# Optimization experiments

Measured on AMD Instinct MI355X. Metric: run time of the kernel, lower is better.

The kernel has to match this reference:

```python
import jax, jax.numpy as jnp
import numpy as np

FP, DP, K, S, B, T, H, ZD = 96, 28, 3, 4, 64, 8, 512, 2
CP = FP - DP + 1          # 69, valid cross-correlation output size
NP = CP * CP              # 4761 = num_pixels


def setup_inputs() -> dict:
    key = jax.random.key(0)
    ks = jax.random.split(key, 12)
    def rn(k, shape, s=0.02):
        return jax.random.normal(k, shape, jnp.float32) * s
    return {
        "frames": jax.random.uniform(ks[0], (S, B, T, FP, FP), jnp.float32),
        "conv_kernel": jax.random.uniform(ks[1], (S, B, K, DP, DP), jnp.float32),
        "eps": jax.random.normal(ks[2], (S, B, K, ZD), jnp.float32),
        "W1": rn(ks[3], (NP, H)), "b1": jnp.zeros((H,), jnp.float32),
        "Wm1": rn(ks[4], (H, H // 2)), "bm1": jnp.zeros((H // 2,), jnp.float32),
        "Wm2": rn(ks[5], (H // 2, ZD)), "bm2": jnp.zeros((ZD,), jnp.float32),
        "Ws1": rn(ks[6], (H, H // 2)), "bs1": jnp.zeros((H // 2,), jnp.float32),
        "Ws2": rn(ks[7], (H // 2, ZD)), "bs2": jnp.zeros((ZD,), jnp.float32),
        "timestep": 0,
    }


def _axis_weights(p, n):
    """Bilinear 1-D gather indices/weights with zero padding outside [0, n)."""
    p0 = jnp.floor(p)
    f = p - p0
    i0 = p0.astype(jnp.int32)
    i1 = i0 + 1
    w0 = jnp.where((i0 >= 0) & (i0 < n), 1.0 - f, 0.0)
    w1 = jnp.where((i1 >= 0) & (i1 < n), f, 0.0)
    return jnp.clip(i0, 0, n - 1), jnp.clip(i1, 0, n - 1), w0, w1


def _place_digit(digit, zw):
    """AT.digit_to_frame: place DPxDP digit into FPxFP frame at z_where (torch
    affine_grid/grid_sample, align_corners=False, zero padding). theta scale =
    FP/DP, translation = -z_where*FP/DP, i.e. in_coord = (FP/DP)*(out - zw)."""
    scale = FP / DP
    out_c = (2.0 * jnp.arange(FP, dtype=jnp.float32) + 1.0) / FP - 1.0  # (FP,)
    px = ((scale * (out_c - zw[0]) + 1.0) * DP - 1.0) * 0.5  # x source pix
    py = ((scale * (out_c - zw[1]) + 1.0) * DP - 1.0) * 0.5  # y source pix
    y0, y1, wy0, wy1 = _axis_weights(py, DP)
    x0, x1, wx0, wx1 = _axis_weights(px, DP)
    # separable bilinear: interp rows then cols
    tmp = wy0[:, None] * digit[y0, :] + wy1[:, None] * digit[y1, :]  # (FP,DP)
    return wx0[None, :] * tmp[:, x0] + wx1[None, :] * tmp[:, x1]     # (FP,FP)

_place_batch = jax.vmap(_place_digit)


def reference(frames, conv_kernel, eps, W1, b1, Wm1, bm1, Wm2, bm2,
              Ws1, bs1, Ws2, bs2, timestep):
    SB = S * B
    frame_left = frames[:, :, timestep]  # (S,B,FP,FP)
    means, stds, zs = [], [], []
    for k in range(K):
        # per-sample dynamic-kernel cross-correlation via grouped conv
        lhs = frame_left.reshape(1, SB, FP, FP)
        rhs = conv_kernel[:, :, k].reshape(SB, 1, DP, DP)
        conved = jax.lax.conv_general_dilated(
            lhs, rhs, (1, 1), 'VALID', feature_group_count=SB)  # (1,SB,CP,CP)
        scores = jax.nn.softmax(conved.reshape(S, B, NP), axis=-1)
        h = jax.nn.relu(scores @ W1 + b1)                       # (S,B,H)
        mean_k = jnp.tanh(jax.nn.relu(h @ Wm1 + bm1) @ Wm2 + bm2)
        std_k = jnp.exp(jax.nn.relu(h @ Ws1 + bs1) @ Ws2 + bs2)
        z_k = mean_k + std_k * eps[:, :, k]                     # rsample
        recon = _place_batch(conv_kernel[:, :, k].reshape(SB, DP, DP),
                             z_k.reshape(SB, ZD)).reshape(S, B, FP, FP)
        frame_left = frame_left - recon
        means.append(mean_k); stds.append(std_k); zs.append(z_k)
    q_mean = jnp.stack(means, 2)    # (S,B,K,2)
    q_std = jnp.stack(stds, 2)
    z_where = jnp.stack(zs, 2)
    return jnp.stack([q_mean, q_std, z_where], 0)  # (3,S,B,K,2)
```

## Files before the change

kernel.cpp:

```cpp
#include <hip/hip_runtime.h>
#include <hip/hip_bf16.h>
#include <math.h>

#define FPD 96
#define DPD 28
#define CPD 69
#define NPD 4761
#define KKC 3
#define SBN 256
#define TT 8
#define HD 512
#define ZDD 2
#define KPAD 4768
#define SPLITK 15
#define FRSH 104
#define CVS 76

typedef __attribute__((ext_vector_type(8))) short bf16x8;
typedef __attribute__((ext_vector_type(4))) float f32x4;
typedef _Float16 half_t;
typedef __attribute__((ext_vector_type(2))) _Float16 half2_t;

__device__ __forceinline__ float bf2f_lo(unsigned int u) {
    union { unsigned int i; float f; } v; v.i = u << 16; return v.f;
}
__device__ __forceinline__ float bf2f_hi(unsigned int u) {
    union { unsigned int i; float f; } v; v.i = u & 0xffff0000u; return v.f;
}
__device__ __forceinline__ half2_t u2h(unsigned int u) {
    union { unsigned int i; half2_t h; } v; v.i = u; return v.h;
}

struct ConvLds {
    half_t fr[96 * FRSH];
    half_t kr[28 * 32];
    float  dg[784];
    float  cv[4][69 * CVS];
    float  red[32];
};

struct MlpLds {
    float hsh[HD];
    float h2[2][256];
    float res_sh[2][2];
};

__device__ __forceinline__ void conv_rest(
    ConvLds& L, int k, int ib, int t,
    const float* __restrict__ pf,
    float* __restrict__ frameL,
    float zx, float zy,
    ushort* __restrict__ e_buf, float* __restrict__ inv_denom)
{
    half_t* fr  = L.fr;
    half_t* kr  = L.kr;
    float*  dg  = L.dg;
    float*  red = L.red;

    const float scale = 96.f / 28.f;
    #pragma unroll
    for (int i = 0; i < 9; ++i) {
        int p = t + i * 1024;
        int r = p / 96, c = p - r * 96;
        float val = pf[i];
        if (k > 0) {
            float oci = (2.f * r + 1.f) / 96.f - 1.f;
            float ocj = (2.f * c + 1.f) / 96.f - 1.f;
            float py = ((scale * (oci - zy) + 1.f) * 28.f - 1.f) * 0.5f;
            float px = ((scale * (ocj - zx) + 1.f) * 28.f - 1.f) * 0.5f;
            float py0f = floorf(py), px0f = floorf(px);
            float fy = py - py0f, fx = px - px0f;
            int y0 = (int)py0f, x0 = (int)px0f;
            int y1 = y0 + 1, x1 = x0 + 1;
            float wy0 = (y0 >= 0 && y0 < DPD) ? 1.f - fy : 0.f;
            float wy1 = (y1 >= 0 && y1 < DPD) ? fy : 0.f;
            float wx0 = (x0 >= 0 && x0 < DPD) ? 1.f - fx : 0.f;
            float wx1 = (x1 >= 0 && x1 < DPD) ? fx : 0.f;
            int y0c = min(max(y0, 0), DPD - 1), y1c = min(max(y1, 0), DPD - 1);
            int x0c = min(max(x0, 0), DPD - 1), x1c = min(max(x1, 0), DPD - 1);
            float tmp0 = wy0 * dg[y0c * DPD + x0c] + wy1 * dg[y1c * DPD + x0c];
            float tmp1 = wy0 * dg[y0c * DPD + x1c] + wy1 * dg[y1c * DPD + x1c];
            val -= wx0 * tmp0 + wx1 * tmp1;
        }
        fr[r * FRSH + c] = (half_t)val;
        if (k == 1) frameL[(size_t)ib * 9216 + p] = val;
    }
    if (t < 96 * 8) fr[(t >> 3) * FRSH + 96 + (t & 7)] = (half_t)0.f;
    __syncthreads();

    if (t < 828) {
        const int q    = t / 207;
        const int rem  = t - q * 207;
        const int tile = rem / 69;
        const int oy   = rem - tile * 69;
        const int ox0  = tile * 24;
        const int dy0  = q * 7;

        float acc[24];
        #pragma unroll
        for (int j = 0; j < 24; ++j) acc[j] = 0.f;

        #pragma unroll 1
        for (int dd = 0; dd < 7; ++dd) {
            const int dy = dy0 + dd;
            const unsigned int* frow = (const unsigned int*)&fr[(oy + dy) * FRSH + ox0];
            const unsigned int* krow = (const unsigned int*)&kr[dy * 32];
            unsigned int W[28], K[16], V[25];
            #pragma unroll
            for (int u = 0; u < 7; ++u) {
                uint4 v = *(const uint4*)(frow + 4 * u);
                W[4*u] = v.x; W[4*u+1] = v.y; W[4*u+2] = v.z; W[4*u+3] = v.w;
            }
            #pragma unroll
            for (int u = 0; u < 4; ++u) {
                uint4 v = *(const uint4*)(krow + 4 * u);
                K[4*u] = v.x; K[4*u+1] = v.y; K[4*u+2] = v.z; K[4*u+3] = v.w;
            }
            #pragma unroll
            for (int i = 0; i < 25; ++i)
                V[i] = (W[i] >> 16) | (W[i + 1] << 16);
            #pragma unroll
            for (int m = 0; m < 12; ++m) {
                float ae = acc[2*m], ao = acc[2*m+1];
                #pragma unroll
                for (int i = 0; i < 14; ++i) {
                    ae = __builtin_amdgcn_fdot2(u2h(W[m + i]), u2h(K[i]), ae, false);
                    ao = __builtin_amdgcn_fdot2(u2h(V[m + i]), u2h(K[i]), ao, false);
                }
                acc[2*m] = ae; acc[2*m+1] = ao;
            }
        }
        float* cvq = &L.cv[q][oy * CVS + ox0];
        #pragma unroll
        for (int u = 0; u < 6; ++u) {
            float4 v = make_float4(acc[4*u], acc[4*u+1], acc[4*u+2], acc[4*u+3]);
            *(float4*)(cvq + 4 * u) = v;
        }
    }
    __syncthreads();

    float m = -INFINITY;
    for (int p = t; p < 69 * CVS; p += 1024) {
        int ox = p - (p / CVS) * CVS;
        if (ox < CPD) {
            float v = L.cv[0][p] + L.cv[1][p] + L.cv[2][p] + L.cv[3][p];
            L.cv[0][p] = v;
            m = fmaxf(m, v);
        }
    }
    #pragma unroll
    for (int off = 32; off > 0; off >>= 1) m = fmaxf(m, __shfl_down(m, off, 64));
    int lane = t & 63, wid = t >> 6;
    if (lane == 0) red[wid] = m;
    __syncthreads();
    m = red[0];
    #pragma unroll
    for (int i = 1; i < 16; ++i) m = fmaxf(m, red[i]);

    float s = 0.f;
    ushort* eo = e_buf + (size_t)ib * KPAD;
    for (int p = t; p < 69 * CVS; p += 1024) {
        int oy = p / CVS;
        int ox = p - oy * CVS;
        if (ox < CPD) {
            float ev = __expf(L.cv[0][p] - m);
            __hip_bfloat16 h = __float2bfloat16(ev);
            eo[oy * CPD + ox] = *reinterpret_cast<ushort*>(&h);
            s += ev;
        }
    }
    #pragma unroll
    for (int off = 32; off > 0; off >>= 1) s += __shfl_down(s, off, 64);
    if (lane == 0) red[16 + wid] = s;
    __syncthreads();
    if (t == 0) {
        float tot = 0.f;
        #pragma unroll
        for (int i = 0; i < 16; ++i) tot += red[16 + i];
        inv_denom[ib] = 1.0f / tot;
    }
    if (t < KPAD - NPD) eo[NPD + t] = 0;
}

__device__ __forceinline__ void mlp_phase(
    MlpLds& L, int km, int ib, int t,
    float csum, float invd, float b1v,
    const ushort* __restrict__ WhidT,
    const float* __restrict__ bm1, const float* __restrict__ bs1,
    const float* __restrict__ Wm2, const float* __restrict__ bm2,
    const float* __restrict__ Ws2, const float* __restrict__ bs2,
    const float* __restrict__ eps, float* __restrict__ out,
    float* z_keep)
{
    if (t < HD)
        L.hsh[t] = fmaxf(fmaf(csum, invd, b1v), 0.f);
    __syncthreads();

    if (t < 512) {
        int head = t >> 8, col = t & 255;
        const uint4* Wr = (const uint4*)(WhidT + (size_t)(head * 256 + col) * 512);
        float bias = head ? bs1[col] : bm1[col];
        float a = 0.f;
        #pragma unroll 8
        for (int u = 0; u < 64; ++u) {
            uint4 wv = Wr[u];
            const float* hp = &L.hsh[u * 8];
            a = fmaf(hp[0], bf2f_lo(wv.x), a);
            a = fmaf(hp[1], bf2f_hi(wv.x), a);
            a = fmaf(hp[2], bf2f_lo(wv.y), a);
            a = fmaf(hp[3], bf2f_hi(wv.y), a);
            a = fmaf(hp[4], bf2f_lo(wv.z), a);
            a = fmaf(hp[5], bf2f_hi(wv.z), a);
            a = fmaf(hp[6], bf2f_lo(wv.w), a);
            a = fmaf(hp[7], bf2f_hi(wv.w), a);
        }
        L.h2[head][col] = fmaxf(a + bias, 0.f);
    }
    __syncthreads();

    {
        int w = t >> 6, l = t & 63;
        if (w < 4) {
            int zd = (w >> 1) & 1, head = w & 1;
            const float* W2 = head ? Ws2 : Wm2;
            float a = 0.f;
            #pragma unroll
            for (int u = 0; u < 4; ++u) {
                int i = l + u * 64;
                a = fmaf(L.h2[head][i], W2[i * 2 + zd], a);
            }
            #pragma unroll
            for (int off = 32; off > 0; off >>= 1) a += __shfl_down(a, off, 64);
            if (l == 0) {
                float r = head ? __expf(a + bs2[zd]) : tanhf(a + bm2[zd]);
                L.res_sh[zd][head] = r;
            }
        }
    }
    __syncthreads();
    if (t < 2) {
        int zd = t;
        float mean = L.res_sh[zd][0];
        float stdv = L.res_sh[zd][1];
        float ev = eps[(size_t)ib * 6 + km * 2 + zd];
        float z = fmaf(stdv, ev, mean);
        int oidx = ib * 6 + km * 2 + zd;
        out[oidx]        = mean;
        out[1536 + oidx] = stdv;
        out[3072 + oidx] = z;
        z_keep[zd] = z;
    }
}

__global__
__attribute__((amdgpu_flat_work_group_size(1024, 1024)))
__attribute__((amdgpu_waves_per_eu(4, 4)))
void conv0_wprep_kernel(
    const float* __restrict__ frames, const int* __restrict__ tsp,
    float* __restrict__ frameL, const float* __restrict__ ck,
    ushort* __restrict__ e_buf, float* __restrict__ inv_denom,
    const float* __restrict__ W1, const float* __restrict__ Wm1,
    const float* __restrict__ Ws1,
    ushort* __restrict__ W1T, ushort* __restrict__ WhidT)
{
    __shared__ union __align__(16) {
        ConvLds conv;
        ushort wp[4][64][65];
    } sh;
    const int t  = threadIdx.x;
    const int ib = blockIdx.x;

    const float* src = frames + ((size_t)ib * TT + *tsp) * 9216;
    float pf[9];
    #pragma unroll
    for (int i = 0; i < 9; ++i) pf[i] = src[t + i * 1024];
    if (t < 28 * 32) {
        int dy = t >> 5, dx = t & 31;
        float v = (dx < 28) ? ck[((size_t)ib * KKC + 0) * 784 + dy * 28 + dx] : 0.f;
        sh.conv.kr[t] = (half_t)v;
    }

    conv_rest(sh.conv, 0, ib, t, pf, frameL, 0.f, 0.f, e_buf, inv_denom);
    __syncthreads();

    {
        const int g  = t >> 8;
        const int tt = t & 255;
        const int ln = tt & 63;
        const int lr = tt >> 6;
        const int b  = ib * 4 + g;
        ushort (*tile)[65] = sh.wp[g];

        if (b < 600) {
            const int k0 = (b % 75) * 64;
            const int n0 = (b / 75) * 64;
            #pragma unroll
            for (int i = 0; i < 16; ++i) {
                int kk = k0 + lr + i * 4;
                float v = (kk < NPD) ? W1[(size_t)kk * HD + n0 + ln] : 0.f;
                __hip_bfloat16 h = __float2bfloat16(v);
                tile[lr + i * 4][ln] = *reinterpret_cast<ushort*>(&h);
            }
        } else if (b < 664) {
            const int bb = b - 600;
            const int i0 = (bb & 7) * 64;
            const int r0 = (bb >> 3) * 64;
            #pragma unroll
            for (int rep = 0; rep < 16; ++rep) {
                int i = i0 + lr + rep * 4;
                int r = r0 + ln;
                const float* srcp = (r >= 256) ? Ws1 : Wm1;
                float v = srcp[(size_t)i * 256 + (r & 255)];
                __hip_bfloat16 h = __float2bfloat16(v);
                tile[lr + rep * 4][ln] = *reinterpret_cast<ushort*>(&h);
            }
        }
        __syncthreads();
        if (b < 600) {
            const int k0 = (b % 75) * 64;
            const int n0 = (b / 75) * 64;
            #pragma unroll
            for (int i = 0; i < 16; ++i) {
                int nn = lr + i * 4;
                int kk = k0 + ln;
                if (kk < KPAD)
                    W1T[(size_t)(n0 + nn) * KPAD + kk] = tile[ln][nn];
            }
        } else if (b < 664) {
            const int bb = b - 600;
            const int i0 = (bb & 7) * 64;
            const int r0 = (bb >> 3) * 64;
            #pragma unroll
            for (int rep = 0; rep < 16; ++rep) {
                int r = r0 + lr + rep * 4;
                WhidT[(size_t)r * 512 + i0 + ln] = tile[ln][lr + rep * 4];
            }
        }
    }
}

__global__ __launch_bounds__(256) void gemm1_mfma(
    const ushort* __restrict__ E, const ushort* __restrict__ W1T,
    float* __restrict__ Cpart)
{
    const int t  = threadIdx.x;
    const int m0 = blockIdx.x * 64;
    const int n0 = blockIdx.y * 64;
    const int z  = blockIdx.z;
    const int step0 = z * 10;
    const int nstep = min(10, 149 - step0);

    const int l  = t & 63;
    const int w  = t >> 6;
    const int lm = l & 15;
    const int kb = l >> 4;

    f32x4 zero = {0.f, 0.f, 0.f, 0.f};
    f32x4 acc[4] = {zero, zero, zero, zero};

    const ushort* pA = E   + (size_t)(m0 + w * 16 + lm) * KPAD + kb * 8;
    const ushort* pB = W1T + (size_t)(n0 + lm) * KPAD + kb * 8;

    int kk = step0 * 32;
    bf16x8 a  = *(const bf16x8*)(pA + kk);
    bf16x8 b0 = *(const bf16x8*)(pB + kk);
    bf16x8 b1 = *(const bf16x8*)(pB + 16 * KPAD + kk);
    bf16x8 b2 = *(const bf16x8*)(pB + 32 * KPAD + kk);
    bf16x8 b3 = *(const bf16x8*)(pB + 48 * KPAD + kk);

    for (int s = 0; s < nstep; ++s) {
        bf16x8 ca = a, c0 = b0, c1 = b1, c2 = b2, c3 = b3;
        if (s + 1 < nstep) {
            kk += 32;
            a  = *(const bf16x8*)(pA + kk);
            b0 = *(const bf16x8*)(pB + kk);
            b1 = *(const bf16x8*)(pB + 16 * KPAD + kk);
            b2 = *(const bf16x8*)(pB + 32 * KPAD + kk);
            b3 = *(const bf16x8*)(pB + 48 * KPAD + kk);
        }
        acc[0] = __builtin_amdgcn_mfma_f32_16x16x32_bf16(ca, c0, acc[0], 0, 0, 0);
        acc[1] = __builtin_amdgcn_mfma_f32_16x16x32_bf16(ca, c1, acc[1], 0, 0, 0);
        acc[2] = __builtin_amdgcn_mfma_f32_16x16x32_bf16(ca, c2, acc[2], 0, 0, 0);
        acc[3] = __builtin_amdgcn_mfma_f32_16x16x32_bf16(ca, c3, acc[3], 0, 0, 0);
    }

    const int mrow = m0 + w * 16 + kb * 4;
    #pragma unroll
    for (int j = 0; j < 4; ++j) {
        int n = n0 + j * 16 + lm;
        #pragma unroll
        for (int rg = 0; rg < 4; ++rg)
            Cpart[((size_t)(mrow + rg) * SPLITK + z) * HD + n] = acc[j][rg];
    }
}

__global__
__attribute__((amdgpu_flat_work_group_size(1024, 1024)))
__attribute__((amdgpu_waves_per_eu(4, 4)))
void mlp_conv_kernel(
    const float* __restrict__ Cpart, const float* __restrict__ inv_denom,
    const float* __restrict__ b1, const ushort* __restrict__ WhidT,
    const float* __restrict__ bm1, const float* __restrict__ bs1,
    const float* __restrict__ Wm2, const float* __restrict__ bm2,
    const float* __restrict__ Ws2, const float* __restrict__ bs2,
    const float* __restrict__ eps, float* __restrict__ out,
    const float* __restrict__ frames, const int* __restrict__ tsp,
    float* __restrict__ frameL, const float* __restrict__ ck,
    ushort* __restrict__ e_buf, int km)
{
    __shared__ union __align__(16) {
        ConvLds conv;
        MlpLds  mlp;
    } sh;
    __shared__ float z_keep[2];
    const int t  = threadIdx.x;
    const int ib = blockIdx.x;
    const int k  = km + 1;

    const float* src = (k < 2)
        ? frames + ((size_t)ib * TT + *tsp) * 9216
        : frameL + (size_t)ib * 9216;
    float pf[9];
    #pragma unroll
    for (int i = 0; i < 9; ++i) pf[i] = src[t + i * 1024];
    if (t < 28 * 32) {
        int dy = t >> 5, dx = t & 31;
        float v = (dx < 28) ? ck[((size_t)ib * KKC + k) * 784 + dy * 28 + dx] : 0.f;
        sh.conv.kr[t] = (half_t)v;
    }
    if (t < 784) sh.conv.dg[t] = ck[((size_t)ib * KKC + (k - 1)) * 784 + t];
    float csum = 0.f, b1v = 0.f;
    if (t < HD) {
        #pragma unroll
        for (int z = 0; z < SPLITK; ++z)
            csum += Cpart[((size_t)ib * SPLITK + z) * HD + t];
        b1v = b1[t];
    }
    float invd = inv_denom[ib];

    mlp_phase(sh.mlp, km, ib, t, csum, invd, b1v, WhidT,
              bm1, bs1, Wm2, bm2, Ws2, bs2, eps, out, z_keep);
    __syncthreads();

    float zx = z_keep[0], zy = z_keep[1];
    conv_rest(sh.conv, k, ib, t, pf, frameL, zx, zy,
              e_buf, (float*)inv_denom);
}

__global__ __launch_bounds__(512) void mlp_final_kernel(
    const float* __restrict__ Cpart, const float* __restrict__ inv_denom,
    const float* __restrict__ b1, const ushort* __restrict__ WhidT,
    const float* __restrict__ bm1, const float* __restrict__ bs1,
    const float* __restrict__ Wm2, const float* __restrict__ bm2,
    const float* __restrict__ Ws2, const float* __restrict__ bs2,
    const float* __restrict__ eps, float* __restrict__ out)
{
    __shared__ MlpLds L;
    __shared__ float z_keep[2];
    const int t  = threadIdx.x;
    const int ib = blockIdx.x;
    float csum = 0.f, b1v = 0.f;
    if (t < HD) {
        #pragma unroll
        for (int z = 0; z < SPLITK; ++z)
            csum += Cpart[((size_t)ib * SPLITK + z) * HD + t];
        b1v = b1[t];
    }
    float invd = inv_denom[ib];
    mlp_phase(L, 2, ib, t, csum, invd, b1v, WhidT,
              bm1, bs1, Wm2, bm2, Ws2, bs2, eps, out, z_keep);
}

extern "C" void kernel_launch(void* const* d_in, const int* in_sizes, int n_in,
                              void* d_out, int out_size, void* d_ws, size_t ws_size,
                              hipStream_t stream)
{
    const float* frames = (const float*)d_in[0];
    const float* ck     = (const float*)d_in[1];
    const float* eps    = (const float*)d_in[2];
    const float* W1     = (const float*)d_in[3];
    const float* b1     = (const float*)d_in[4];
    const float* Wm1    = (const float*)d_in[5];
    const float* bm1    = (const float*)d_in[6];
    const float* Wm2    = (const float*)d_in[7];
    const float* bm2    = (const float*)d_in[8];
    const float* Ws1    = (const float*)d_in[9];
    const float* bs1    = (const float*)d_in[10];
    const float* Ws2    = (const float*)d_in[11];
    const float* bs2    = (const float*)d_in[12];
    const int*   tsp    = (const int*)d_in[13];
    float* out = (float*)d_out;

    float* frameL  = (float*)d_ws;
    float* Cpart   = frameL + 2359296;
    float* inv_den = Cpart + 1966080;
    ushort* e_buf  = (ushort*)(inv_den + 256);
    ushort* W1T    = e_buf + (size_t)SBN * KPAD;
    ushort* WhidT  = W1T + (size_t)HD * KPAD;

    conv0_wprep_kernel<<<256, 1024, 0, stream>>>(
        frames, tsp, frameL, ck, e_buf, inv_den, W1, Wm1, Ws1, W1T, WhidT);
    gemm1_mfma<<<dim3(4, 8, SPLITK), 256, 0, stream>>>(e_buf, W1T, Cpart);
    mlp_conv_kernel<<<256, 1024, 0, stream>>>(
        Cpart, inv_den, b1, WhidT, bm1, bs1, Wm2, bm2, Ws2, bs2,
        eps, out, frames, tsp, frameL, ck, e_buf, 0);
    gemm1_mfma<<<dim3(4, 8, SPLITK), 256, 0, stream>>>(e_buf, W1T, Cpart);
    mlp_conv_kernel<<<256, 1024, 0, stream>>>(
        Cpart, inv_den, b1, WhidT, bm1, bs1, Wm2, bm2, Ws2, bs2,
        eps, out, frames, tsp, frameL, ck, e_buf, 1);
    gemm1_mfma<<<dim3(4, 8, SPLITK), 256, 0, stream>>>(e_buf, W1T, Cpart);
    mlp_final_kernel<<<256, 512, 0, stream>>>(
        Cpart, inv_den, b1, WhidT, bm1, bs1, Wm2, bm2, Ws2, bs2, eps, out);
}
```

Baseline: 299.2 us.

## Recompute residual frame from prior digits instead of storing it; split gemm blocks into single waves

Stop writing and re-reading the residual frame in workspace. The last conv stage now rebuilds it from the original frame by subtracting both earlier bilinear reconstructions, reading the first z from the output buffer. The conv kernel is templated on the stage so dead branches compile away. The split-K GEMM also moves from 4-wave blocks to single-wave 64-thread blocks (4x more blocks) with a two-deep register prefetch. The trade is about 9 MB less global traffic for extra ALU work and LDS gathers in the last stage.

```diff
diff --git a/kernel.cpp b/kernel.cpp
--- a/kernel.cpp
+++ b/kernel.cpp
@@ -34,7 +34,7 @@
 struct ConvLds {
     half_t fr[96 * FRSH];
     half_t kr[28 * 32];
-    float  dg[784];
+    float  dg[2][784];
     float  cv[4][69 * CVS];
     float  red[32];
 };
@@ -45,45 +45,48 @@
     float res_sh[2][2];
 };
 
+__device__ __forceinline__ float recon_val(
+    const float* __restrict__ dg, float zx, float zy, int r, int c)
+{
+    const float scale = 96.f / 28.f;
+    float oci = (2.f * r + 1.f) / 96.f - 1.f;
+    float ocj = (2.f * c + 1.f) / 96.f - 1.f;
+    float py = ((scale * (oci - zy) + 1.f) * 28.f - 1.f) * 0.5f;
+    float px = ((scale * (ocj - zx) + 1.f) * 28.f - 1.f) * 0.5f;
+    float py0f = floorf(py), px0f = floorf(px);
+    float fy = py - py0f, fx = px - px0f;
+    int y0 = (int)py0f, x0 = (int)px0f;
+    int y1 = y0 + 1, x1 = x0 + 1;
+    float wy0 = (y0 >= 0 && y0 < DPD) ? 1.f - fy : 0.f;
+    float wy1 = (y1 >= 0 && y1 < DPD) ? fy : 0.f;
+    float wx0 = (x0 >= 0 && x0 < DPD) ? 1.f - fx : 0.f;
+    float wx1 = (x1 >= 0 && x1 < DPD) ? fx : 0.f;
+    int y0c = min(max(y0, 0), DPD - 1), y1c = min(max(y1, 0), DPD - 1);
+    int x0c = min(max(x0, 0), DPD - 1), x1c = min(max(x1, 0), DPD - 1);
+    float tmp0 = wy0 * dg[y0c * DPD + x0c] + wy1 * dg[y1c * DPD + x0c];
+    float tmp1 = wy0 * dg[y0c * DPD + x1c] + wy1 * dg[y1c * DPD + x1c];
+    return wx0 * tmp0 + wx1 * tmp1;
+}
+
+template<int NREC>
 __device__ __forceinline__ void conv_rest(
-    ConvLds& L, int k, int ib, int t,
+    ConvLds& L, int ib, int t,
     const float* __restrict__ pf,
-    float* __restrict__ frameL,
-    float zx, float zy,
+    float z0x, float z0y, float z1x, float z1y,
     ushort* __restrict__ e_buf, float* __restrict__ inv_denom)
 {
     half_t* fr  = L.fr;
     half_t* kr  = L.kr;
-    float*  dg  = L.dg;
     float*  red = L.red;
 
-    const float scale = 96.f / 28.f;
     #pragma unroll
     for (int i = 0; i < 9; ++i) {
         int p = t + i * 1024;
         int r = p / 96, c = p - r * 96;
         float val = pf[i];
-        if (k > 0) {
-            float oci = (2.f * r + 1.f) / 96.f - 1.f;
-            float ocj = (2.f * c + 1.f) / 96.f - 1.f;
-            float py = ((scale * (oci - zy) + 1.f) * 28.f - 1.f) * 0.5f;
-            float px = ((scale * (ocj - zx) + 1.f) * 28.f - 1.f) * 0.5f;
-            float py0f = floorf(py), px0f = floorf(px);
-            float fy = py - py0f, fx = px - px0f;
-            int y0 = (int)py0f, x0 = (int)px0f;
-            int y1 = y0 + 1, x1 = x0 + 1;
-            float wy0 = (y0 >= 0 && y0 < DPD) ? 1.f - fy : 0.f;
-            float wy1 = (y1 >= 0 && y1 < DPD) ? fy : 0.f;
-            float wx0 = (x0 >= 0 && x0 < DPD) ? 1.f - fx : 0.f;
-            float wx1 = (x1 >= 0 && x1 < DPD) ? fx : 0.f;
-            int y0c = min(max(y0, 0), DPD - 1), y1c = min(max(y1, 0), DPD - 1);
-            int x0c = min(max(x0, 0), DPD - 1), x1c = min(max(x1, 0), DPD - 1);
-            float tmp0 = wy0 * dg[y0c * DPD + x0c] + wy1 * dg[y1c * DPD + x0c];
-            float tmp1 = wy0 * dg[y0c * DPD + x1c] + wy1 * dg[y1c * DPD + x1c];
-            val -= wx0 * tmp0 + wx1 * tmp1;
-        }
+        if (NREC >= 1) val -= recon_val(L.dg[0], z0x, z0y, r, c);
+        if (NREC >= 2) val -= recon_val(L.dg[1], z1x, z1y, r, c);
         fr[r * FRSH + c] = (half_t)val;
-        if (k == 1) frameL[(size_t)ib * 9216 + p] = val;
     }
     if (t < 96 * 8) fr[(t >> 3) * FRSH + 96 + (t & 7)] = (half_t)0.f;
     __syncthreads();
@@ -257,7 +260,7 @@
 __attribute__((amdgpu_waves_per_eu(4, 4)))
 void conv0_wprep_kernel(
     const float* __restrict__ frames, const int* __restrict__ tsp,
-    float* __restrict__ frameL, const float* __restrict__ ck,
+    const float* __restrict__ ck,
     ushort* __restrict__ e_buf, float* __restrict__ inv_denom,
     const float* __restrict__ W1, const float* __restrict__ Wm1,
     const float* __restrict__ Ws1,
@@ -280,7 +283,7 @@
         sh.conv.kr[t] = (half_t)v;
     }
 
-    conv_rest(sh.conv, 0, ib, t, pf, frameL, 0.f, 0.f, e_buf, inv_denom);
+    conv_rest<0>(sh.conv, ib, t, pf, 0.f, 0.f, 0.f, 0.f, e_buf, inv_denom);
     __syncthreads();
 
     {
@@ -339,52 +342,65 @@
     }
 }
 
-__global__ __launch_bounds__(256) void gemm1_mfma(
+#define GLOADSET(A,B0,B1,B2,B3,OFF)                        \
+    A  = *(const bf16x8*)(pA + (OFF));                     \
+    B0 = *(const bf16x8*)(pB + (OFF));                     \
+    B1 = *(const bf16x8*)(pB + 16 * KPAD + (OFF));         \
+    B2 = *(const bf16x8*)(pB + 32 * KPAD + (OFF));         \
+    B3 = *(const bf16x8*)(pB + 48 * KPAD + (OFF));
+
+__global__ __launch_bounds__(64) void gemm1_mfma(
     const ushort* __restrict__ E, const ushort* __restrict__ W1T,
     float* __restrict__ Cpart)
 {
     const int t  = threadIdx.x;
-    const int m0 = blockIdx.x * 64;
+    const int bx = blockIdx.x;
     const int n0 = blockIdx.y * 64;
     const int z  = blockIdx.z;
     const int step0 = z * 10;
     const int nstep = min(10, 149 - step0);
 
-    const int l  = t & 63;
-    const int w  = t >> 6;
-    const int lm = l & 15;
-    const int kb = l >> 4;
+    const int lm = t & 15;
+    const int kb = (t & 63) >> 4;
 
     f32x4 zero = {0.f, 0.f, 0.f, 0.f};
     f32x4 acc[4] = {zero, zero, zero, zero};
 
-    const ushort* pA = E   + (size_t)(m0 + w * 16 + lm) * KPAD + kb * 8;
+    const ushort* pA = E   + (size_t)(bx * 16 + lm) * KPAD + kb * 8;
     const ushort* pB = W1T + (size_t)(n0 + lm) * KPAD + kb * 8;
-
-    int kk = step0 * 32;
-    bf16x8 a  = *(const bf16x8*)(pA + kk);
-    bf16x8 b0 = *(const bf16x8*)(pB + kk);
-    bf16x8 b1 = *(const bf16x8*)(pB + 16 * KPAD + kk);
-    bf16x8 b2 = *(const bf16x8*)(pB + 32 * KPAD + kk);
-    bf16x8 b3 = *(const bf16x8*)(pB + 48 * KPAD + kk);
-
-    for (int s = 0; s < nstep; ++s) {
-        bf16x8 ca = a, c0 = b0, c1 = b1, c2 = b2, c3 = b3;
-        if (s + 1 < nstep) {
-            kk += 32;
-            a  = *(const bf16x8*)(pA + kk);
-            b0 = *(const bf16x8*)(pB + kk);
-            b1 = *(const bf16x8*)(pB + 16 * KPAD + kk);
-            b2 = *(const bf16x8*)(pB + 32 * KPAD + kk);
-            b3 = *(const bf16x8*)(pB + 48 * KPAD + kk);
-        }
+    const int kk0 = step0 * 32;
+
+    bf16x8 a0, b00, b01, b02, b03;
+    bf16x8 a1, b10, b11, b12, b13;
+    GLOADSET(a0, b00, b01, b02, b03, kk0)
+    GLOADSET(a1, b10, b11, b12, b13, kk0 + 32)
+
+    int s = 0;
+    for (; s + 2 <= nstep; s += 2) {
+        bf16x8 ca = a0, c0 = b00, c1 = b01, c2 = b02, c3 = b03;
+        if (s + 2 < nstep) { int kn = kk0 + (s + 2) * 32;
+            GLOADSET(a0, b00, b01, b02, b03, kn) }
         acc[0] = __builtin_amdgcn_mfma_f32_16x16x32_bf16(ca, c0, acc[0], 0, 0, 0);
         acc[1] = __builtin_amdgcn_mfma_f32_16x16x32_bf16(ca, c1, acc[1], 0, 0, 0);
         acc[2] = __builtin_amdgcn_mfma_f32_16x16x32_bf16(ca, c2, acc[2], 0, 0, 0);
         acc[3] = __builtin_amdgcn_mfma_f32_16x16x32_bf16(ca, c3, acc[3], 0, 0, 0);
-    }
-
-    const int mrow = m0 + w * 16 + kb * 4;
+
+        bf16x8 da = a1, d0 = b10, d1 = b11, d2 = b12, d3 = b13;
+        if (s + 3 < nstep) { int kn = kk0 + (s + 3) * 32;
+            GLOADSET(a1, b10, b11, b12, b13, kn) }
+        acc[0] = __builtin_amdgcn_mfma_f32_16x16x32_bf16(da, d0, acc[0], 0, 0, 0);
+        acc[1] = __builtin_amdgcn_mfma_f32_16x16x32_bf16(da, d1, acc[1], 0, 0, 0);
+        acc[2] = __builtin_amdgcn_mfma_f32_16x16x32_bf16(da, d2, acc[2], 0, 0, 0);
+        acc[3] = __builtin_amdgcn_mfma_f32_16x16x32_bf16(da, d3, acc[3], 0, 0, 0);
+    }
+    if (s < nstep) {
+        acc[0] = __builtin_amdgcn_mfma_f32_16x16x32_bf16(a0, b00, acc[0], 0, 0, 0);
+        acc[1] = __builtin_amdgcn_mfma_f32_16x16x32_bf16(a0, b01, acc[1], 0, 0, 0);
+        acc[2] = __builtin_amdgcn_mfma_f32_16x16x32_bf16(a0, b02, acc[2], 0, 0, 0);
+        acc[3] = __builtin_amdgcn_mfma_f32_16x16x32_bf16(a0, b03, acc[3], 0, 0, 0);
+    }
+
+    const int mrow = bx * 16 + kb * 4;
     #pragma unroll
     for (int j = 0; j < 4; ++j) {
         int n = n0 + j * 16 + lm;
@@ -394,6 +410,7 @@
     }
 }
 
+template<int KM>
 __global__
 __attribute__((amdgpu_flat_work_group_size(1024, 1024)))
 __attribute__((amdgpu_waves_per_eu(4, 4)))
@@ -405,8 +422,7 @@
     const float* __restrict__ Ws2, const float* __restrict__ bs2,
     const float* __restrict__ eps, float* __restrict__ out,
     const float* __restrict__ frames, const int* __restrict__ tsp,
-    float* __restrict__ frameL, const float* __restrict__ ck,
-    ushort* __restrict__ e_buf, int km)
+    const float* __restrict__ ck, ushort* __restrict__ e_buf)
 {
     __shared__ union __align__(16) {
         ConvLds conv;
@@ -415,20 +431,27 @@
     __shared__ float z_keep[2];
     const int t  = threadIdx.x;
     const int ib = blockIdx.x;
-    const int k  = km + 1;
-
-    const float* src = (k < 2)
-        ? frames + ((size_t)ib * TT + *tsp) * 9216
-        : frameL + (size_t)ib * 9216;
+
+    const float* src = frames + ((size_t)ib * TT + *tsp) * 9216;
     float pf[9];
     #pragma unroll
     for (int i = 0; i < 9; ++i) pf[i] = src[t + i * 1024];
     if (t < 28 * 32) {
         int dy = t >> 5, dx = t & 31;
-        float v = (dx < 28) ? ck[((size_t)ib * KKC + k) * 784 + dy * 28 + dx] : 0.f;
+        float v = (dx < 28)
+            ? ck[((size_t)ib * KKC + (KM + 1)) * 784 + dy * 28 + dx] : 0.f;
         sh.conv.kr[t] = (half_t)v;
     }
-    if (t < 784) sh.conv.dg[t] = ck[((size_t)ib * KKC + (k - 1)) * 784 + t];
+    if (t < 784) {
+        sh.conv.dg[0][t] = ck[((size_t)ib * KKC + 0) * 784 + t];
+        if (KM == 1)
+            sh.conv.dg[1][t] = ck[((size_t)ib * KKC + 1) * 784 + t];
+    }
+    float z0x = 0.f, z0y = 0.f;
+    if (KM == 1) {
+        z0x = out[3072 + ib * 6 + 0];
+        z0y = out[3072 + ib * 6 + 1];
+    }
     float csum = 0.f, b1v = 0.f;
     if (t < HD) {
         #pragma unroll
@@ -438,13 +461,18 @@
     }
     float invd = inv_denom[ib];
 
-    mlp_phase(sh.mlp, km, ib, t, csum, invd, b1v, WhidT,
+    mlp_phase(sh.mlp, KM, ib, t, csum, invd, b1v, WhidT,
               bm1, bs1, Wm2, bm2, Ws2, bs2, eps, out, z_keep);
     __syncthreads();
 
-    float zx = z_keep[0], zy = z_keep[1];
-    conv_rest(sh.conv, k, ib, t, pf, frameL, zx, zy,
-              e_buf, (float*)inv_denom);
+    float zkx = z_keep[0], zky = z_keep[1];
+    if (KM == 0) {
+        conv_rest<1>(sh.conv, ib, t, pf, zkx, zky, 0.f, 0.f,
+                     e_buf, (float*)inv_denom);
+    } else {
+        conv_rest<2>(sh.conv, ib, t, pf, z0x, z0y, zkx, zky,
+                     e_buf, (float*)inv_denom);
+    }
 }
 
 __global__ __launch_bounds__(512) void mlp_final_kernel(
@@ -491,24 +519,23 @@
     const int*   tsp    = (const int*)d_in[13];
     float* out = (float*)d_out;
 
-    float* frameL  = (float*)d_ws;
-    float* Cpart   = frameL + 2359296;
+    float* Cpart   = (float*)d_ws;
     float* inv_den = Cpart + 1966080;
     ushort* e_buf  = (ushort*)(inv_den + 256);
     ushort* W1T    = e_buf + (size_t)SBN * KPAD;
     ushort* WhidT  = W1T + (size_t)HD * KPAD;
 
     conv0_wprep_kernel<<<256, 1024, 0, stream>>>(
-        frames, tsp, frameL, ck, e_buf, inv_den, W1, Wm1, Ws1, W1T, WhidT);
-    gemm1_mfma<<<dim3(4, 8, SPLITK), 256, 0, stream>>>(e_buf, W1T, Cpart);
-    mlp_conv_kernel<<<256, 1024, 0, stream>>>(
+        frames, tsp, ck, e_buf, inv_den, W1, Wm1, Ws1, W1T, WhidT);
+    gemm1_mfma<<<dim3(16, 8, SPLITK), 64, 0, stream>>>(e_buf, W1T, Cpart);
+    mlp_conv_kernel<0><<<256, 1024, 0, stream>>>(
         Cpart, inv_den, b1, WhidT, bm1, bs1, Wm2, bm2, Ws2, bs2,
-        eps, out, frames, tsp, frameL, ck, e_buf, 0);
-    gemm1_mfma<<<dim3(4, 8, SPLITK), 256, 0, stream>>>(e_buf, W1T, Cpart);
-    mlp_conv_kernel<<<256, 1024, 0, stream>>>(
+        eps, out, frames, tsp, ck, e_buf);
+    gemm1_mfma<<<dim3(16, 8, SPLITK), 64, 0, stream>>>(e_buf, W1T, Cpart);
+    mlp_conv_kernel<1><<<256, 1024, 0, stream>>>(
         Cpart, inv_den, b1, WhidT, bm1, bs1, Wm2, bm2, Ws2, bs2,
-        eps, out, frames, tsp, frameL, ck, e_buf, 1);
-    gemm1_mfma<<<dim3(4, 8, SPLITK), 256, 0, stream>>>(e_buf, W1T, Cpart);
+        eps, out, frames, tsp, ck, e_buf);
+    gemm1_mfma<<<dim3(16, 8, SPLITK), 64, 0, stream>>>(e_buf, W1T, Cpart);
     mlp_final_kernel<<<256, 512, 0, stream>>>(
         Cpart, inv_den, b1, WhidT, bm1, bs1, Wm2, bm2, Ws2, bs2, eps, out);
 }
```

Result: slower. 305.3 us (+2.0%).
